# Optimization experiments

Measured on AMD Instinct MI355X. Metric: run time of the kernel, lower is better.

Reference implementation:

```python
import math
import jax, jax.numpy as jnp
import numpy as np

B, N, D, H, P = 16, 500, 32, 128, 100
E = N * D
N_HEADS, QKV = 8, 16
TANH_CLIP = 10.0

def setup_inputs() -> dict:
    key = jax.random.key(0)
    ks = jax.random.split(key, 16)
    emb = jax.random.normal(ks[0], (B, E, H), jnp.float32)
    dists = jax.random.uniform(ks[1], (B, N, N, 2), jnp.float32)
    pref = jax.random.uniform(ks[2], (2,), jnp.float32)
    # regular edge list: node i owns edges [i*D, (i+1)*D); dst random in [0,N)
    src = jnp.broadcast_to(jnp.arange(E, dtype=jnp.int32) // D, (B, E))
    dst = jax.random.randint(ks[3], (B, E), 0, N, dtype=jnp.int32)
    indices = jnp.stack([src, dst], axis=-1)
    w = lambda k: jax.random.normal(k, (H, H), jnp.float32) * 0.05
    return {
        'embeddings': emb,
        'dists': dists,
        'pref': pref,
        'indices': indices,
        'Wq_first': w(ks[4]), 'Wq_last': w(ks[5]), 'Wq_visited': w(ks[6]),
        'Wq_graph': w(ks[7]), 'Wq': w(ks[8]), 'Wk': w(ks[9]),
        'q_first': jax.random.normal(ks[10], (B, P, H), jnp.float32),
        'visited_embedding': jnp.zeros((B, P, H), jnp.float32),
        'last_edge_embedding': jax.random.normal(ks[11], (B, P, H), jnp.float32),
        'last_node_index': jax.random.randint(ks[12], (B, P), 0, N, dtype=jnp.int32),
        'group_ninf_mask': jnp.zeros((B, P, N), jnp.float32),
    }

def reference(embeddings, dists, pref, indices, Wq_first, Wq_last, Wq_visited,
              Wq_graph, Wq, Wk, q_first, visited_embedding, last_edge_embedding,
              last_node_index, group_ninf_mask):
    Bsz, Etot, Hd = embeddings.shape
    Nn = dists.shape[1]
    Deg = Etot // Nn
    # combined objective (training_method == 'Linear')
    dists_c = pref[0] * dists[..., 0] + pref[1] * dists[..., 1]  # [B,N,N]
    # outgoing edge ids of each current node (regular degree -> contiguous block)
    out_idx = last_node_index[:, :, None].astype(jnp.int32) * Deg + jnp.arange(Deg, dtype=jnp.int32)  # [B,P,D]
    bidx = jnp.arange(Bsz)[:, None, None]
    outgoing_embeddings = embeddings[bidx, out_idx]          # [B,P,D,H]
    node_keys = indices[bidx, out_idx, 1]                    # [B,P,D] dst nodes
    # queries (q_first already set -> add_more_query path)
    q_graph = jnp.mean(embeddings, axis=1, keepdims=True) @ Wq_graph.T   # [B,1,H]
    q_last = last_edge_embedding @ Wq_last.T                 # [B,P,H]
    visited = visited_embedding + last_edge_embedding / Nn
    q_visited = visited @ Wq_visited.T
    final_q = q_last + q_first + q_graph + q_visited         # [B,P,H]
    # multi-head pointer attention over the D outgoing edges
    k = (outgoing_embeddings @ Wk.T).reshape(Bsz, -1, Deg, N_HEADS, QKV)   # [B,P,D,h,q]
    qh = (final_q @ Wq.T).reshape(Bsz, -1, N_HEADS, QKV)                    # [B,P,h,q]
    score = jnp.einsum('bpdhq,bphq->bhpd', k, qh) / math.sqrt(Hd)           # [B,h,P,D]
    distances = dists_c[jnp.arange(Bsz)[:, None], last_node_index]          # [B,P,N]
    d_sorted = jnp.take_along_axis(distances, node_keys, axis=2)            # [B,P,D]
    score = score - (d_sorted / math.sqrt(2.0))[:, None]
    score_clipped = TANH_CLIP * jnp.tanh(score.mean(axis=1))                # [B,P,D] (multi_pointer_level==1)
    mask = jnp.take_along_axis(group_ninf_mask, node_keys, axis=2)
    mask = jnp.where(jnp.isneginf(mask), jnp.float32(-1e8), mask)
    probs = jax.nn.softmax(score_clipped + mask, axis=-1)
    return probs, node_keys, outgoing_embeddings
```

## Files before the change

### kernel.cpp

```cpp
#include <hip/hip_runtime.h>
#include <hip/hip_bf16.h>
#include <math.h>

#define Bsz 16
#define Nn  500
#define Deg 32
#define Hd  128
#define Pg  100
#define Etot 16000
#define CHUNKS 64
#define ROWS_PER_CHUNK 250
#define PREP_BLKS 256

__global__ __launch_bounds__(256) void fused_all(const float* __restrict__ emb,
                                                 const float* __restrict__ wq,
                                                 const float* __restrict__ wk,
                                                 const float* __restrict__ wql,
                                                 const float* __restrict__ wqv,
                                                 const float* __restrict__ wqg,
                                                 float* __restrict__ partial,
                                                 float* __restrict__ mt,
                                                 float* __restrict__ at,
                                                 float* __restrict__ bt,
                                                 float* __restrict__ gt) {
    int blk = blockIdx.x;
    int tid = threadIdx.x;
    __shared__ float4 red[256];
    __shared__ float wv_s[2][Hd];

    if (blk >= PREP_BLKS) {
        int mb = blk - PREP_BLKS;
        int b = mb >> 6, chunk = mb & 63;
        int rgrp = tid >> 5, c4 = tid & 31;
        const float4* base = (const float4*)(emb + (size_t)b * Etot * Hd);
        int e0 = chunk * ROWS_PER_CHUNK;
        float4 acc = make_float4(0.f, 0.f, 0.f, 0.f);
        for (int e = e0 + rgrp; e < e0 + ROWS_PER_CHUNK; e += 8) {
            float4 v = base[(size_t)e * 32 + c4];
            acc.x += v.x; acc.y += v.y; acc.z += v.z; acc.w += v.w;
        }
        red[tid] = acc;
        __syncthreads();
        for (int s = 128; s >= 32; s >>= 1) {
            if (tid < s) {
                float4 a = red[tid], o = red[tid + s];
                a.x += o.x; a.y += o.y; a.z += o.z; a.w += o.w;
                red[tid] = a;
            }
            __syncthreads();
        }
        if (tid < 32)
            ((float4*)partial)[((size_t)b * CHUNKS + chunk) * 32 + tid] = red[tid];
        return;
    }

    int h = tid >> 7;
    int r = tid & 127;
    if (blk < 64) {
        int s = (blk << 1) | h;
        float acc = 0.f;
#pragma unroll 8
        for (int t = 0; t < Hd; ++t)
            acc += wq[t * Hd + s] * wk[t * Hd + r];
        mt[s * Hd + r] = acc;
        return;
    }
    int f = (blk - 64) >> 6;
    int u = (((blk - 64) & 63) << 1) | h;
    int t = r;
    float acc1 = 0.f;
    if (f == 0) {
#pragma unroll 8
        for (int s = 0; s < Hd; ++s)
            acc1 += (wql[s * Hd + u] + wqv[s * Hd + u] * (1.f / (float)Nn)) * wq[t * Hd + s];
    } else if (f == 1) {
#pragma unroll 8
        for (int s = 0; s < Hd; ++s)
            acc1 += wqv[s * Hd + u] * wq[t * Hd + s];
    } else {
#pragma unroll 8
        for (int s = 0; s < Hd; ++s)
            acc1 += wqg[s * Hd + u] * wq[t * Hd + s];
    }
    wv_s[h][t] = acc1;
    __syncthreads();
    float acc = 0.f;
#pragma unroll 8
    for (int tt = 0; tt < Hd; ++tt)
        acc += wv_s[h][tt] * wk[tt * Hd + r];
    float* dst = (f == 0) ? at : (f == 1) ? bt : gt;
    dst[u * Hd + r] = acc;
}

__global__ __launch_bounds__(256) void decode_z(const float* __restrict__ partial,
                                                const float* __restrict__ gt,
                                                const float* __restrict__ at,
                                                const float* __restrict__ bt,
                                                const float* __restrict__ mt,
                                                const float* __restrict__ qf,
                                                const float* __restrict__ vis,
                                                const float* __restrict__ le,
                                                const float* __restrict__ emb,
                                                const float* __restrict__ dists,
                                                const float* __restrict__ pref,
                                                const int* __restrict__ indices,
                                                const int* __restrict__ lni_arr,
                                                const float* __restrict__ gmask,
                                                float* __restrict__ out_probs,
                                                float* __restrict__ out_nk,
                                                float* __restrict__ out_og) {
    int blk = blockIdx.x;
    int b = blk / 25, p0 = (blk % 25) * 4;
    int bp0 = b * Pg + p0;
    int tid = threadIdx.x;

    __shared__ int lni_s[4];
    __shared__ float ps[2][Hd];
    __shared__ float mean_s[Hd];
    __shared__ __align__(16) float ins[Hd][3][4];
    __shared__ float zpart[2][4][Hd];
    __shared__ __align__(16) float z_s[4][Hd];
    __shared__ float score_s[4][Deg];

    if (tid < 4) lni_s[tid] = lni_arr[bp0 + tid];
    __syncthreads();

    int bp_i = tid >> 5, d = tid & 31;
    int nk = 0; float2 dd = make_float2(0.f, 0.f); float mval = 0.f;
    if (tid < 128) {
        int lnv = lni_s[bp_i];
        nk = indices[(((size_t)b * Etot) + (size_t)lnv * Deg + d) * 2 + 1];
        out_nk[(size_t)(bp0 + bp_i) * Deg + d] = (float)nk;
        dd = *(const float2*)(dists + (((size_t)b * Nn + (size_t)lnv) * Nn + nk) * 2);
        mval = gmask[(size_t)(bp0 + bp_i) * Nn + nk];
    }
    float p0v = pref[0], p1v = pref[1];

    {
        int c = tid & 127, h = tid >> 7;
        float s = 0.f;
        const float* pb = partial + (size_t)b * CHUNKS * Hd;
        for (int k = h * 32; k < h * 32 + 32; ++k)
            s += pb[k * Hd + c];
        ps[h][c] = s;
    }
    {
        size_t base4 = (size_t)bp0 * 32;
        const float4* le4 = (const float4*)le + base4;
        const float4* vi4 = (const float4*)vis + base4;
        const float4* qf4 = (const float4*)qf + base4;
        for (int i = tid; i < 384; i += 256) {
            int m = i >> 7, idx = i & 127;
            int bp = idx >> 5, c4 = idx & 31;
            float4 v = (m == 0) ? le4[idx] : (m == 1) ? vi4[idx] : qf4[idx];
            int u0 = c4 * 4;
            ins[u0 + 0][m][bp] = v.x;
            ins[u0 + 1][m][bp] = v.y;
            ins[u0 + 2][m][bp] = v.z;
            ins[u0 + 3][m][bp] = v.w;
        }
    }
    __syncthreads();
    if (tid < Hd)
        mean_s[tid] = (ps[0][tid] + ps[1][tid]) * (1.f / (float)Etot);
    __syncthreads();

    {
        int r = tid & 127, h = tid >> 7;
        float acc0 = 0.f, acc1 = 0.f, acc2 = 0.f, acc3 = 0.f, accg = 0.f;
        const float* atp = at + r;
        const float* btp = bt + r;
        const float* mtp = mt + r;
        const float* gtp = gt + r;
#pragma unroll 4
        for (int u = h * 64; u < h * 64 + 64; ++u) {
            float wa = atp[u * Hd];
            float wb = btp[u * Hd];
            float wm = mtp[u * Hd];
            float wg = gtp[u * Hd];
            accg += wg * mean_s[u];
            float4 lv = *(const float4*)&ins[u][0][0];
            float4 vv = *(const float4*)&ins[u][1][0];
            float4 qv = *(const float4*)&ins[u][2][0];
            acc0 += wa * lv.x + wb * vv.x + wm * qv.x;
            acc1 += wa * lv.y + wb * vv.y + wm * qv.y;
            acc2 += wa * lv.z + wb * vv.z + wm * qv.z;
            acc3 += wa * lv.w + wb * vv.w + wm * qv.w;
        }
        zpart[h][0][r] = acc0 + accg;
        zpart[h][1][r] = acc1 + accg;
        zpart[h][2][r] = acc2 + accg;
        zpart[h][3][r] = acc3 + accg;
    }
    __syncthreads();
    for (int i = tid; i < 512; i += 256) {
        int bp = i >> 7, r = i & 127;
        z_s[bp][r] = zpart[0][bp][r] + zpart[1][bp][r];
    }
    __syncthreads();

    {
        int rg = tid >> 5, c4 = tid & 31;
        for (int bp = 0; bp < 4; ++bp) {
            const float4* ebase = (const float4*)emb + ((size_t)b * Etot + (size_t)lni_s[bp] * Deg) * 32;
            float4* ob = (float4*)out_og + ((size_t)(bp0 + bp)) * (Deg * 32);
            float4 z4 = ((const float4*)z_s[bp])[c4];
#pragma unroll
            for (int r0 = 0; r0 < 4; ++r0) {
                int r = rg + r0 * 8;
                float4 v = ebase[r * 32 + c4];
                ob[r * 32 + c4] = v;
                float part = v.x * z4.x + v.y * z4.y + v.z * z4.z + v.w * z4.w;
                for (int m = 16; m >= 1; m >>= 1)
                    part += __shfl_xor(part, m, 64);
                if (c4 == 0) score_s[bp][r] = part;
            }
        }
    }
    __syncthreads();

    if (tid < 128) {
        float s = score_s[bp_i][d] * 0.011048543456039805f;
        float ds = p0v * dd.x + p1v * dd.y;
        s -= ds * 0.7071067811865476f;
        float sc = 10.0f * tanhf(s);
        float m = mval;
        if (isinf(m) && m < 0.f) m = -1.0e8f;
        float v = sc + m;
        float mx = v;
        for (int mm = 16; mm >= 1; mm >>= 1)
            mx = fmaxf(mx, __shfl_xor(mx, mm, 64));
        float e = expf(v - mx);
        float sum = e;
        for (int mm = 16; mm >= 1; mm >>= 1)
            sum += __shfl_xor(sum, mm, 64);
        out_probs[(size_t)(bp0 + bp_i) * Deg + d] = e / sum;
    }
}

extern "C" void kernel_launch(void* const* d_in, const int* in_sizes, int n_in,
                              void* d_out, int out_size, void* d_ws, size_t ws_size,
                              hipStream_t stream) {
    const float* emb       = (const float*)d_in[0];
    const float* dists     = (const float*)d_in[1];
    const float* pref      = (const float*)d_in[2];
    const int*   indices   = (const int*)d_in[3];
    const float* Wq_last    = (const float*)d_in[5];
    const float* Wq_visited = (const float*)d_in[6];
    const float* Wq_graph   = (const float*)d_in[7];
    const float* Wq         = (const float*)d_in[8];
    const float* Wk         = (const float*)d_in[9];
    const float* q_first    = (const float*)d_in[10];
    const float* visited    = (const float*)d_in[11];
    const float* last_edge  = (const float*)d_in[12];
    const int*   lni        = (const int*)d_in[13];
    const float* gmask      = (const float*)d_in[14];

    float* w = (float*)d_ws;
    float* ws_partial = w;
    float* ws_mt      = ws_partial + (size_t)Bsz * CHUNKS * Hd;
    float* ws_at      = ws_mt + Hd * Hd;
    float* ws_bt      = ws_at + Hd * Hd;
    float* ws_gt      = ws_bt + Hd * Hd;

    float* out       = (float*)d_out;
    float* out_probs = out;
    float* out_nk    = out + (size_t)Bsz * Pg * Deg;
    float* out_og    = out + 2 * (size_t)Bsz * Pg * Deg;

    fused_all<<<PREP_BLKS + Bsz * CHUNKS, 256, 0, stream>>>(emb, Wq, Wk, Wq_last, Wq_visited,
                                                            Wq_graph, ws_partial, ws_mt,
                                                            ws_at, ws_bt, ws_gt);
    decode_z<<<400, 256, 0, stream>>>(ws_partial, ws_gt, ws_at, ws_bt, ws_mt,
                                      q_first, visited, last_edge, emb, dists, pref,
                                      indices, lni, gmask, out_probs, out_nk, out_og);
}
```

Measured before the change: 48.54 us.

## Move outgoing-embedding gather and node-key writes into the first kernel

The copy of outgoing edge embeddings and the node-key output writes move out of the decode kernel and into 1600 extra blocks of the first kernel, which do not depend on any prep results. This spreads the large output write (about 26 MB) across the first launch, overlapping it with the mean reduction and weight-prep blocks, and shortens the decode kernel's critical path. The decode kernel still re-reads the same embedding rows for scoring, so embedding reads are now done twice, and the first kernel has more blocks.

```diff
diff --git a/kernel.cpp b/kernel.cpp
--- a/kernel.cpp
+++ b/kernel.cpp
@@ -10,26 +10,52 @@
 #define Etot 16000
 #define CHUNKS 64
 #define ROWS_PER_CHUNK 250
-#define PREP_BLKS 256
-
-__global__ __launch_bounds__(256) void fused_all(const float* __restrict__ emb,
-                                                 const float* __restrict__ wq,
-                                                 const float* __restrict__ wk,
-                                                 const float* __restrict__ wql,
-                                                 const float* __restrict__ wqv,
-                                                 const float* __restrict__ wqg,
-                                                 float* __restrict__ partial,
-                                                 float* __restrict__ mt,
-                                                 float* __restrict__ at,
-                                                 float* __restrict__ bt,
-                                                 float* __restrict__ gt) {
+#define NB_PREP 256
+#define NB_MEAN (Bsz * CHUNKS)
+#define NB_OG   (Bsz * Pg)
+
+__global__ __launch_bounds__(256) void mega1(const float* __restrict__ emb,
+                                             const float* __restrict__ wq,
+                                             const float* __restrict__ wk,
+                                             const float* __restrict__ wql,
+                                             const float* __restrict__ wqv,
+                                             const float* __restrict__ wqg,
+                                             const int* __restrict__ indices,
+                                             const int* __restrict__ lni_arr,
+                                             float* __restrict__ partial,
+                                             float* __restrict__ mt,
+                                             float* __restrict__ at,
+                                             float* __restrict__ bt,
+                                             float* __restrict__ gt,
+                                             float* __restrict__ out_nk,
+                                             float* __restrict__ out_og) {
     int blk = blockIdx.x;
     int tid = threadIdx.x;
+
+    if (blk >= NB_PREP + NB_MEAN) {
+        int bp = blk - (NB_PREP + NB_MEAN);
+        int b = bp / Pg;
+        int lni = lni_arr[bp];
+        if (tid < Deg) {
+            int nk = indices[(((size_t)b * Etot) + (size_t)lni * Deg + tid) * 2 + 1];
+            out_nk[(size_t)bp * Deg + tid] = (float)nk;
+        }
+        const float4* ebase = (const float4*)(emb) + ((size_t)b * Etot + (size_t)lni * Deg) * 32;
+        float4* obase = (float4*)(out_og) + (size_t)bp * Deg * 32;
+        int grp = tid >> 5, c4 = tid & 31;
+#pragma unroll
+        for (int r = 0; r < 4; ++r) {
+            int rr = grp + r * 8;
+            obase[rr * 32 + c4] = ebase[rr * 32 + c4];
+        }
+        return;
+    }
+
     __shared__ float4 red[256];
     __shared__ float wv_s[2][Hd];
 
-    if (blk >= PREP_BLKS) {
-        int mb = blk - PREP_BLKS;
+    if (blk >= NB_PREP) {
+        int mb = blk - NB_PREP;
         int b = mb >> 6, chunk = mb & 63;
         int rgrp = tid >> 5, c4 = tid & 31;
         const float4* base = (const float4*)(emb + (size_t)b * Etot * Hd);
@@ -106,9 +132,7 @@
                                                 const int* __restrict__ indices,
                                                 const int* __restrict__ lni_arr,
                                                 const float* __restrict__ gmask,
-                                                float* __restrict__ out_probs,
-                                                float* __restrict__ out_nk,
-                                                float* __restrict__ out_og) {
+                                                float* __restrict__ out_probs) {
     int blk = blockIdx.x;
     int b = blk / 25, p0 = (blk % 25) * 4;
     int bp0 = b * Pg + p0;
@@ -130,7 +154,6 @@
     if (tid < 128) {
         int lnv = lni_s[bp_i];
         nk = indices[(((size_t)b * Etot) + (size_t)lnv * Deg + d) * 2 + 1];
-        out_nk[(size_t)(bp0 + bp_i) * Deg + d] = (float)nk;
         dd = *(const float2*)(dists + (((size_t)b * Nn + (size_t)lnv) * Nn + nk) * 2);
         mval = gmask[(size_t)(bp0 + bp_i) * Nn + nk];
     }
@@ -203,13 +226,11 @@
         int rg = tid >> 5, c4 = tid & 31;
         for (int bp = 0; bp < 4; ++bp) {
             const float4* ebase = (const float4*)emb + ((size_t)b * Etot + (size_t)lni_s[bp] * Deg) * 32;
-            float4* ob = (float4*)out_og + ((size_t)(bp0 + bp)) * (Deg * 32);
             float4 z4 = ((const float4*)z_s[bp])[c4];
 #pragma unroll
             for (int r0 = 0; r0 < 4; ++r0) {
                 int r = rg + r0 * 8;
                 float4 v = ebase[r * 32 + c4];
-                ob[r * 32 + c4] = v;
                 float part = v.x * z4.x + v.y * z4.y + v.z * z4.z + v.w * z4.w;
                 for (int m = 16; m >= 1; m >>= 1)
                     part += __shfl_xor(part, m, 64);
@@ -268,10 +289,11 @@
     float* out_nk    = out + (size_t)Bsz * Pg * Deg;
     float* out_og    = out + 2 * (size_t)Bsz * Pg * Deg;
 
-    fused_all<<<PREP_BLKS + Bsz * CHUNKS, 256, 0, stream>>>(emb, Wq, Wk, Wq_last, Wq_visited,
-                                                            Wq_graph, ws_partial, ws_mt,
-                                                            ws_at, ws_bt, ws_gt);
+    mega1<<<NB_PREP + NB_MEAN + NB_OG, 256, 0, stream>>>(emb, Wq, Wk, Wq_last, Wq_visited,
+                                                         Wq_graph, indices, lni, ws_partial,
+                                                         ws_mt, ws_at, ws_bt, ws_gt,
+                                                         out_nk, out_og);
     decode_z<<<400, 256, 0, stream>>>(ws_partial, ws_gt, ws_at, ws_bt, ws_mt,
                                       q_first, visited, last_edge, emb, dists, pref,
-                                      indices, lni, gmask, out_probs, out_nk, out_og);
+                                      indices, lni, gmask, out_probs);
 }
```

After: 53.78 us. +10.8%, slower.

## Compute per-query z vectors directly instead of precomputing fused weight products

Applied to the files above, without the earlier changes.

Drops the precomputed weight-product matrices (Wq^T·Wk and the last, visited and graph variants) except the graph one. The first kernel gains 400 blocks that, for each group of four queries, apply Wq_last and Wq_visited, then Wq, then Wk using shared-memory weight tiles, and write a z vector per query. decode_z now only adds the graph term to the loaded z vector. This removes the 128x128x128 weight-product work, at the cost of reloading the weight matrices in every block and adding many block barriers.

```diff
diff --git a/kernel.cpp b/kernel.cpp
--- a/kernel.cpp
+++ b/kernel.cpp
@@ -10,26 +10,30 @@
 #define Etot 16000
 #define CHUNKS 64
 #define ROWS_PER_CHUNK 250
-#define PREP_BLKS 256
-
-__global__ __launch_bounds__(256) void fused_all(const float* __restrict__ emb,
-                                                 const float* __restrict__ wq,
-                                                 const float* __restrict__ wk,
-                                                 const float* __restrict__ wql,
-                                                 const float* __restrict__ wqv,
-                                                 const float* __restrict__ wqg,
-                                                 float* __restrict__ partial,
-                                                 float* __restrict__ mt,
-                                                 float* __restrict__ at,
-                                                 float* __restrict__ bt,
-                                                 float* __restrict__ gt) {
+#define NB_Z1   400
+#define NB_GT   64
+#define NB_MEAN (Bsz * CHUNKS)
+#define TILE 16
+
+__global__ __launch_bounds__(256) void mega1(const float* __restrict__ emb,
+                                             const float* __restrict__ wq,
+                                             const float* __restrict__ wk,
+                                             const float* __restrict__ wql,
+                                             const float* __restrict__ wqv,
+                                             const float* __restrict__ wqg,
+                                             const float* __restrict__ qf,
+                                             const float* __restrict__ vis,
+                                             const float* __restrict__ le,
+                                             float* __restrict__ partial,
+                                             float* __restrict__ gt,
+                                             float* __restrict__ z1g) {
+    __shared__ __align__(16) char smem[18496];
     int blk = blockIdx.x;
     int tid = threadIdx.x;
-    __shared__ float4 red[256];
-    __shared__ float wv_s[2][Hd];
-
-    if (blk >= PREP_BLKS) {
-        int mb = blk - PREP_BLKS;
+
+    if (blk >= NB_Z1 + NB_GT) {
+        float4* red = (float4*)smem;
+        int mb = blk - (NB_Z1 + NB_GT);
         int b = mb >> 6, chunk = mb & 63;
         int rgrp = tid >> 5, c4 = tid & 31;
         const float4* base = (const float4*)(emb + (size_t)b * Etot * Hd);
@@ -54,52 +58,114 @@
         return;
     }
 
-    int h = tid >> 7;
-    int r = tid & 127;
-    if (blk < 64) {
-        int s = (blk << 1) | h;
+    if (blk >= NB_Z1) {
+        float (*wv_s)[Hd] = (float (*)[Hd])smem;
+        int h = tid >> 7, r = tid & 127;
+        int u = (((blk - NB_Z1)) << 1) | h;
+        float acc1 = 0.f;
+#pragma unroll 8
+        for (int s = 0; s < Hd; ++s)
+            acc1 += wqg[s * Hd + u] * wq[r * Hd + s];
+        wv_s[h][r] = acc1;
+        __syncthreads();
         float acc = 0.f;
 #pragma unroll 8
-        for (int t = 0; t < Hd; ++t)
-            acc += wq[t * Hd + s] * wk[t * Hd + r];
-        mt[s * Hd + r] = acc;
+        for (int tt = 0; tt < Hd; ++tt)
+            acc += wv_s[h][tt] * wk[tt * Hd + r];
+        gt[u * Hd + r] = acc;
         return;
     }
-    int f = (blk - 64) >> 6;
-    int u = (((blk - 64) & 63) << 1) | h;
-    int t = r;
-    float acc1 = 0.f;
-    if (f == 0) {
-#pragma unroll 8
-        for (int s = 0; s < Hd; ++s)
-            acc1 += (wql[s * Hd + u] + wqv[s * Hd + u] * (1.f / (float)Nn)) * wq[t * Hd + s];
-    } else if (f == 1) {
-#pragma unroll 8
-        for (int s = 0; s < Hd; ++s)
-            acc1 += wqv[s * Hd + u] * wq[t * Hd + s];
-    } else {
-#pragma unroll 8
-        for (int s = 0; s < Hd; ++s)
-            acc1 += wqg[s * Hd + u] * wq[t * Hd + s];
-    }
-    wv_s[h][t] = acc1;
-    __syncthreads();
-    float acc = 0.f;
-#pragma unroll 8
-    for (int tt = 0; tt < Hd; ++tt)
-        acc += wv_s[h][tt] * wk[tt * Hd + r];
-    float* dst = (f == 0) ? at : (f == 1) ? bt : gt;
-    dst[u * Hd + r] = acc;
+
+    {
+        float* wt   = (float*)smem;
+        float* le_s = wt + TILE * 129;
+        float* vi_s = le_s + 512;
+        float* qf_s = vi_s + 512;
+        float* fq_s = qf_s + 512;
+        float* qh_s = fq_s + 512;
+
+        int unit = blk;
+        int b = unit / 25, p0 = (unit % 25) * 4;
+        int bp0 = b * Pg + p0;
+
+        for (int i = tid; i < 512; i += 256) {
+            int bp = i >> 7, c = i & 127;
+            size_t off = (size_t)(bp0 + bp) * Hd + c;
+            float l = le[off];
+            le_s[i] = l;
+            vi_s[i] = vis[off] + l * (1.f / (float)Nn);
+            qf_s[i] = qf[off];
+        }
+        __syncthreads();
+
+        int t = tid & 127, g = tid >> 7;
+        int x0o = (2 * g) * 128, x1o = (2 * g + 1) * 128;
+
+        float a0 = 0.f, a1 = 0.f;
+        for (int k = 0; k < Hd / TILE; ++k) {
+            for (int i = tid; i < Hd * TILE; i += 256) {
+                int row = i >> 4, s = i & (TILE - 1);
+                wt[s * 129 + row] = wql[row * Hd + k * TILE + s];
+            }
+            __syncthreads();
+#pragma unroll
+            for (int s = 0; s < TILE; ++s) {
+                float w = wt[s * 129 + t];
+                a0 += w * le_s[x0o + k * TILE + s];
+                a1 += w * le_s[x1o + k * TILE + s];
+            }
+            __syncthreads();
+            for (int i = tid; i < Hd * TILE; i += 256) {
+                int row = i >> 4, s = i & (TILE - 1);
+                wt[s * 129 + row] = wqv[row * Hd + k * TILE + s];
+            }
+            __syncthreads();
+#pragma unroll
+            for (int s = 0; s < TILE; ++s) {
+                float w = wt[s * 129 + t];
+                a0 += w * vi_s[x0o + k * TILE + s];
+                a1 += w * vi_s[x1o + k * TILE + s];
+            }
+            __syncthreads();
+        }
+        fq_s[x0o + t] = a0 + qf_s[x0o + t];
+        fq_s[x1o + t] = a1 + qf_s[x1o + t];
+        __syncthreads();
+
+        a0 = a1 = 0.f;
+        for (int k = 0; k < Hd / TILE; ++k) {
+            for (int i = tid; i < Hd * TILE; i += 256) {
+                int row = i >> 4, s = i & (TILE - 1);
+                wt[s * 129 + row] = wq[row * Hd + k * TILE + s];
+            }
+            __syncthreads();
+#pragma unroll
+            for (int s = 0; s < TILE; ++s) {
+                float w = wt[s * 129 + t];
+                a0 += w * fq_s[x0o + k * TILE + s];
+                a1 += w * fq_s[x1o + k * TILE + s];
+            }
+            __syncthreads();
+        }
+        qh_s[x0o + t] = a0;
+        qh_s[x1o + t] = a1;
+        __syncthreads();
+
+        float z0 = 0.f, z1a = 0.f;
+#pragma unroll 4
+        for (int u = 0; u < Hd; ++u) {
+            float w = wk[u * Hd + t];
+            z0  += w * qh_s[x0o + u];
+            z1a += w * qh_s[x1o + u];
+        }
+        z1g[(size_t)(bp0 + 2 * g) * Hd + t]     = z0;
+        z1g[(size_t)(bp0 + 2 * g + 1) * Hd + t] = z1a;
+    }
 }
 
 __global__ __launch_bounds__(256) void decode_z(const float* __restrict__ partial,
                                                 const float* __restrict__ gt,
-                                                const float* __restrict__ at,
-                                                const float* __restrict__ bt,
-                                                const float* __restrict__ mt,
-                                                const float* __restrict__ qf,
-                                                const float* __restrict__ vis,
-                                                const float* __restrict__ le,
+                                                const float* __restrict__ z1g,
                                                 const float* __restrict__ emb,
                                                 const float* __restrict__ dists,
                                                 const float* __restrict__ pref,
@@ -117,8 +183,7 @@
     __shared__ int lni_s[4];
     __shared__ float ps[2][Hd];
     __shared__ float mean_s[Hd];
-    __shared__ __align__(16) float ins[Hd][3][4];
-    __shared__ float zpart[2][4][Hd];
+    __shared__ float gzp[2][Hd];
     __shared__ __align__(16) float z_s[4][Hd];
     __shared__ float score_s[4][Deg];
 
@@ -144,22 +209,6 @@
             s += pb[k * Hd + c];
         ps[h][c] = s;
     }
-    {
-        size_t base4 = (size_t)bp0 * 32;
-        const float4* le4 = (const float4*)le + base4;
-        const float4* vi4 = (const float4*)vis + base4;
-        const float4* qf4 = (const float4*)qf + base4;
-        for (int i = tid; i < 384; i += 256) {
-            int m = i >> 7, idx = i & 127;
-            int bp = idx >> 5, c4 = idx & 31;
-            float4 v = (m == 0) ? le4[idx] : (m == 1) ? vi4[idx] : qf4[idx];
-            int u0 = c4 * 4;
-            ins[u0 + 0][m][bp] = v.x;
-            ins[u0 + 1][m][bp] = v.y;
-            ins[u0 + 2][m][bp] = v.z;
-            ins[u0 + 3][m][bp] = v.w;
-        }
-    }
     __syncthreads();
     if (tid < Hd)
         mean_s[tid] = (ps[0][tid] + ps[1][tid]) * (1.f / (float)Etot);
@@ -167,35 +216,17 @@
 
     {
         int r = tid & 127, h = tid >> 7;
-        float acc0 = 0.f, acc1 = 0.f, acc2 = 0.f, acc3 = 0.f, accg = 0.f;
-        const float* atp = at + r;
-        const float* btp = bt + r;
-        const float* mtp = mt + r;
+        float acc = 0.f;
         const float* gtp = gt + r;
 #pragma unroll 4
-        for (int u = h * 64; u < h * 64 + 64; ++u) {
-            float wa = atp[u * Hd];
-            float wb = btp[u * Hd];
-            float wm = mtp[u * Hd];
-            float wg = gtp[u * Hd];
-            accg += wg * mean_s[u];
-            float4 lv = *(const float4*)&ins[u][0][0];
-            float4 vv = *(const float4*)&ins[u][1][0];
-            float4 qv = *(const float4*)&ins[u][2][0];
-            acc0 += wa * lv.x + wb * vv.x + wm * qv.x;
-            acc1 += wa * lv.y + wb * vv.y + wm * qv.y;
-            acc2 += wa * lv.z + wb * vv.z + wm * qv.z;
-            acc3 += wa * lv.w + wb * vv.w + wm * qv.w;
-        }
-        zpart[h][0][r] = acc0 + accg;
-        zpart[h][1][r] = acc1 + accg;
-        zpart[h][2][r] = acc2 + accg;
-        zpart[h][3][r] = acc3 + accg;
+        for (int u = h * 64; u < h * 64 + 64; ++u)
+            acc += gtp[u * Hd] * mean_s[u];
+        gzp[h][r] = acc;
     }
     __syncthreads();
     for (int i = tid; i < 512; i += 256) {
         int bp = i >> 7, r = i & 127;
-        z_s[bp][r] = zpart[0][bp][r] + zpart[1][bp][r];
+        z_s[bp][r] = z1g[(size_t)(bp0 + bp) * Hd + r] + gzp[0][r] + gzp[1][r];
     }
     __syncthreads();
 
@@ -258,20 +289,17 @@
 
     float* w = (float*)d_ws;
     float* ws_partial = w;
-    float* ws_mt      = ws_partial + (size_t)Bsz * CHUNKS * Hd;
-    float* ws_at      = ws_mt + Hd * Hd;
-    float* ws_bt      = ws_at + Hd * Hd;
-    float* ws_gt      = ws_bt + Hd * Hd;
+    float* ws_gt      = ws_partial + (size_t)Bsz * CHUNKS * Hd;
+    float* ws_z1      = ws_gt + Hd * Hd;
 
     float* out       = (float*)d_out;
     float* out_probs = out;
     float* out_nk    = out + (size_t)Bsz * Pg * Deg;
     float* out_og    = out + 2 * (size_t)Bsz * Pg * Deg;
 
-    fused_all<<<PREP_BLKS + Bsz * CHUNKS, 256, 0, stream>>>(emb, Wq, Wk, Wq_last, Wq_visited,
-                                                            Wq_graph, ws_partial, ws_mt,
-                                                            ws_at, ws_bt, ws_gt);
-    decode_z<<<400, 256, 0, stream>>>(ws_partial, ws_gt, ws_at, ws_bt, ws_mt,
-                                      q_first, visited, last_edge, emb, dists, pref,
+    mega1<<<NB_Z1 + NB_GT + NB_MEAN, 256, 0, stream>>>(emb, Wq, Wk, Wq_last, Wq_visited,
+                                                       Wq_graph, q_first, visited, last_edge,
+                                                       ws_partial, ws_gt, ws_z1);
+    decode_z<<<400, 256, 0, stream>>>(ws_partial, ws_gt, ws_z1, emb, dists, pref,
                                       indices, lni, gmask, out_probs, out_nk, out_og);
 }
```

Result: slower. 111.0 us (+128.7%).
